# Kernel optimization log

Hardware: AMD Instinct MI355X
Metric: run time of the kernel (lower is better)

## Reference

```python
import jax, jax.numpy as jnp
import numpy as np

EMBED = 1024
HEADS = 16
HEAD_DIM = EMBED // HEADS
FFN = 4096
B, S = 2, 2048
EPS = 1e-5


def setup_inputs() -> dict:
    key = jax.random.key(0)
    ks = jax.random.split(key, 16)
    sc = 0.02
    return {
        "x": jax.random.normal(ks[0], (B, S, EMBED), jnp.float32),
        "rope_cos": jax.random.uniform(ks[1], (S, HEAD_DIM), jnp.float32),
        "rope_sin": jax.random.uniform(ks[2], (S, HEAD_DIM), jnp.float32),
        "Wq": jax.random.normal(ks[3], (EMBED, EMBED), jnp.float32) * sc,
        "bq": jnp.zeros((EMBED,), jnp.float32),
        "Wk": jax.random.normal(ks[4], (EMBED, EMBED), jnp.float32) * sc,
        "bk": jnp.zeros((EMBED,), jnp.float32),
        "Wv": jax.random.normal(ks[5], (EMBED, EMBED), jnp.float32) * sc,
        "bv": jnp.zeros((EMBED,), jnp.float32),
        "Wo": jax.random.normal(ks[6], (EMBED, EMBED), jnp.float32) * sc,
        "bo": jnp.zeros((EMBED,), jnp.float32),
        "W1": jax.random.normal(ks[7], (EMBED, FFN), jnp.float32) * sc,
        "b1": jnp.zeros((FFN,), jnp.float32),
        "W2": jax.random.normal(ks[8], (FFN, EMBED), jnp.float32) * sc,
        "b2": jnp.zeros((EMBED,), jnp.float32),
        "g1": jnp.ones((EMBED,), jnp.float32),
        "be1": jnp.zeros((EMBED,), jnp.float32),
        "g2": jnp.ones((EMBED,), jnp.float32),
        "be2": jnp.zeros((EMBED,), jnp.float32),
    }


def _layernorm(x, g, b):
    mu = jnp.mean(x, axis=-1, keepdims=True)
    var = jnp.var(x, axis=-1, keepdims=True)
    return (x - mu) * jax.lax.rsqrt(var + EPS) * g + b


def _rotate_half(x):
    half = x.shape[-1] // 2
    return jnp.concatenate((-x[..., half:], x[..., :half]), axis=-1)


def _apply_rope(x, cos, sin):
    # x: (B, H, S, D); cos/sin: (S, D)
    return x * cos[None, None] + _rotate_half(x) * sin[None, None]


def reference(x, rope_cos, rope_sin, Wq, bq, Wk, bk, Wv, bv, Wo, bo,
              W1, b1, W2, b2, g1, be1, g2, be2):
    batch, seq_len, embed = x.shape
    n = _layernorm(x, g1, be1)

    def heads(t):
        return t.reshape(batch, seq_len, HEADS, HEAD_DIM).transpose(0, 2, 1, 3)

    q = heads(n @ Wq + bq)
    k = heads(n @ Wk + bk)
    v = heads(n @ Wv + bv)
    q = _apply_rope(q, rope_cos, rope_sin)
    k = _apply_rope(k, rope_cos, rope_sin)

    scale = 1.0 / np.sqrt(HEAD_DIM)
    scores = jnp.einsum("bhqd,bhkd->bhqk", q, k) * scale  # (B,H,S,S)
    causal = jnp.triu(jnp.ones((seq_len, seq_len), bool), k=1)
    scores = jnp.where(causal[None, None], -jnp.inf, scores)
    attn = jax.nn.softmax(scores, axis=-1)
    out = jnp.einsum("bhqk,bhkd->bhqd", attn, v)
    out = out.transpose(0, 2, 1, 3).reshape(batch, seq_len, embed)
    x = x + (out @ Wo + bo)

    n2 = _layernorm(x, g2, be2)
    h = jax.nn.gelu(n2 @ W1 + b1, approximate=False)
    x = x + (h @ W2 + b2)
    return x
```

## Files before the change

### kernel.cpp

```cpp
#include <hip/hip_runtime.h>
#include <math.h>

#define EMBED 1024
#define SLEN  2048
#define BATCH 2
#define HEADS 16
#define HD    64
#define FFN_D 4096
#define MROWS (BATCH*SLEN)

typedef short bh8  __attribute__((ext_vector_type(8)));
typedef float f32x4 __attribute__((ext_vector_type(4)));

#define MFMA16(a,b,c) __builtin_amdgcn_mfma_f32_16x16x32_bf16((a),(b),(c),0,0,0)
#define GLDS16(g,l) __builtin_amdgcn_global_load_lds( \
    (__attribute__((address_space(1))) void*)(g), \
    (__attribute__((address_space(3))) void*)(l), 16, 0, 0)

__device__ inline float b2f(short s) {
  union { unsigned u; float f; } c; c.u = ((unsigned)(unsigned short)s) << 16; return c.f;
}
__device__ inline short f2b(float f) {
  union { float f; unsigned u; } c; c.f = f;
  unsigned r = (c.u + 0x7FFFu + ((c.u >> 16) & 1u)) >> 16;
  return (short)r;
}

__global__ __launch_bounds__(256) void transpose_w(const float* __restrict__ in,
                                                   short* __restrict__ out,
                                                   int K, int N) {
  __shared__ short sm[64][65];
  const int tid = threadIdx.x;
  const int k0 = blockIdx.y * 64, n0 = blockIdx.x * 64;
#pragma unroll
  for (int it = 0; it < 16; ++it) {
    int idx = it * 256 + tid;
    int r = idx >> 6, c = idx & 63;
    sm[r][c] = f2b(in[(size_t)(k0 + r) * N + n0 + c]);
  }
  __syncthreads();
#pragma unroll
  for (int it = 0; it < 16; ++it) {
    int idx = it * 256 + tid;
    int r = idx >> 6, c = idx & 63;
    out[(size_t)(n0 + r) * K + k0 + c] = sm[c][r];
  }
}

__global__ __launch_bounds__(256) void transpose_v(const short* __restrict__ in,
                                                   short* __restrict__ out) {
  __shared__ short sm[64][65];
  const int tid = threadIdx.x;
  const int s0 = blockIdx.x * 64, bh = blockIdx.y;
  const int b = bh >> 4, h = bh & 15;
#pragma unroll
  for (int it = 0; it < 16; ++it) {
    int idx = it * 256 + tid;
    int r = idx >> 6, c = idx & 63;
    sm[r][c] = in[((size_t)(b*SLEN + s0 + r))*EMBED + h*HD + c];
  }
  __syncthreads();
#pragma unroll
  for (int it = 0; it < 16; ++it) {
    int idx = it * 256 + tid;
    int r = idx >> 6, c = idx & 63;
    out[((size_t)(bh*HD + r))*SLEN + s0 + c] = sm[c][r];
  }
}

__global__ __launch_bounds__(256) void ln_kernel(const float* __restrict__ inF,
                                                 const short* __restrict__ inB,
                                                 const float* __restrict__ gw,
                                                 const float* __restrict__ bw,
                                                 short* __restrict__ out) {
  const int row = blockIdx.x, tid = threadIdx.x;
  const int w = tid >> 6;
  const size_t base = (size_t)row * EMBED;
  float x[4];
#pragma unroll
  for (int i = 0; i < 4; ++i) {
    int c = tid + i * 256;
    x[i] = inF ? inF[base + c] : b2f(inB[base + c]);
  }
  float s = x[0] + x[1] + x[2] + x[3];
  float ss = x[0]*x[0] + x[1]*x[1] + x[2]*x[2] + x[3]*x[3];
#pragma unroll
  for (int off = 32; off >= 1; off >>= 1) { s += __shfl_xor(s, off); ss += __shfl_xor(ss, off); }
  __shared__ float red[8];
  if ((tid & 63) == 0) { red[w*2] = s; red[w*2+1] = ss; }
  __syncthreads();
  s  = red[0] + red[2] + red[4] + red[6];
  ss = red[1] + red[3] + red[5] + red[7];
  const float mu = s * (1.0f/EMBED);
  const float var = ss * (1.0f/EMBED) - mu*mu;
  const float rstd = rsqrtf(var + 1e-5f);
#pragma unroll
  for (int i = 0; i < 4; ++i) {
    int c = tid + i * 256;
    out[base + c] = f2b((x[i]-mu)*rstd*gw[c] + bw[c]);
  }
}

__global__ __launch_bounds__(256) void rope_kernel(short* __restrict__ Qb, short* __restrict__ Kb,
                                                   const float* __restrict__ cosb,
                                                   const float* __restrict__ sinb) {
  const int idx = blockIdx.x * 256 + threadIdx.x;
  const int d = idx & 31;
  const int h = (idx >> 5) & 15;
  const int s = (idx >> 9) & 2047;
  const int b = idx >> 20;
  const size_t base = ((size_t)(b*SLEN + s))*EMBED + h*HD;
  const float c0 = cosb[s*HD + d],      s0 = sinb[s*HD + d];
  const float c1 = cosb[s*HD + 32 + d], s1 = sinb[s*HD + 32 + d];
  float q0 = b2f(Qb[base + d]), q1 = b2f(Qb[base + 32 + d]);
  Qb[base + d]      = f2b(q0*c0 - q1*s0);
  Qb[base + 32 + d] = f2b(q1*c1 + q0*s1);
  float k0 = b2f(Kb[base + d]), k1 = b2f(Kb[base + 32 + d]);
  Kb[base + d]      = f2b(k0*c0 - k1*s0);
  Kb[base + 32 + d] = f2b(k1*c1 + k0*s1);
}

__global__ __launch_bounds__(256) void gemm_bt(const short* __restrict__ A,
                                               const short* __restrict__ Bt,
                                               const float* __restrict__ bias0,
                                               const float* __restrict__ bias1,
                                               const float* __restrict__ bias2,
                                               float* __restrict__ outF,
                                               short* __restrict__ outB0,
                                               short* __restrict__ outB1,
                                               short* __restrict__ outB2,
                                               const float* __restrict__ residF,
                                               const short* __restrict__ residB,
                                               int N, int K, int gelu, int qkv) {
  __shared__ short As[128*32];
  __shared__ short Bs[128*32];
  const int tid = threadIdx.x;
  const int w = tid >> 6, L = tid & 63;
  const int quad = L >> 4, l16 = L & 15;
  const int bm = blockIdx.y * 128, bn = blockIdx.x * 128;
  const int wm = (w >> 1) * 64, wn = (w & 1) * 64;

  f32x4 acc[4][4];
#pragma unroll
  for (int i = 0; i < 4; ++i)
#pragma unroll
    for (int j = 0; j < 4; ++j) acc[i][j] = (f32x4){0.f,0.f,0.f,0.f};

  const int c0 = w*64 + L, c1 = 256 + w*64 + L;
  const short* a0p = A  + (size_t)(bm + (c0 >> 2))*K + (c0 & 3)*8;
  const short* a1p = A  + (size_t)(bm + (c1 >> 2))*K + (c1 & 3)*8;
  const short* b0p = Bt + (size_t)(bn + (c0 >> 2))*K + (c0 & 3)*8;
  const short* b1p = Bt + (size_t)(bn + (c1 >> 2))*K + (c1 & 3)*8;

  for (int k0 = 0; k0 < K; k0 += 32) {
    GLDS16(a0p + k0, As + w*512);
    GLDS16(a1p + k0, As + 2048 + w*512);
    GLDS16(b0p + k0, Bs + w*512);
    GLDS16(b1p + k0, Bs + 2048 + w*512);
    __syncthreads();
    bh8 af[4], bf[4];
#pragma unroll
    for (int mi = 0; mi < 4; ++mi)
      af[mi] = *(const bh8*)(As + (wm + mi*16 + l16)*32 + quad*8);
#pragma unroll
    for (int ni = 0; ni < 4; ++ni)
      bf[ni] = *(const bh8*)(Bs + (wn + ni*16 + l16)*32 + quad*8);
#pragma unroll
    for (int mi = 0; mi < 4; ++mi)
#pragma unroll
      for (int ni = 0; ni < 4; ++ni)
        acc[mi][ni] = MFMA16(af[mi], bf[ni], acc[mi][ni]);
    __syncthreads();
  }

#pragma unroll
  for (int mi = 0; mi < 4; ++mi) {
#pragma unroll
    for (int ni = 0; ni < 4; ++ni) {
      const int col = bn + wn + ni*16 + l16;
      float bv; short* ob; int colw; size_t rstride;
      if (qkv) {
        const int cc = col >> 10;
        colw = col & 1023;
        bv = (cc == 0 ? bias0 : cc == 1 ? bias1 : bias2)[colw];
        ob = (cc == 0 ? outB0 : cc == 1 ? outB1 : outB2);
        rstride = 1024;
      } else {
        colw = col; bv = bias0 ? bias0[col] : 0.f; ob = outB0; rstride = N;
      }
#pragma unroll
      for (int r = 0; r < 4; ++r) {
        const int gr = bm + wm + mi*16 + quad*4 + r;
        float v = acc[mi][ni][r] + bv;
        if (gelu) v = 0.5f*v*(1.f + erff(v*0.70710678f));
        if (residF) v += residF[(size_t)gr*N + col];
        if (residB) v += b2f(residB[(size_t)gr*N + col]);
        if (outF) outF[(size_t)gr*N + col] = v;
        if (ob)   ob[(size_t)gr*rstride + colw] = f2b(v);
      }
    }
  }
}

__global__ __launch_bounds__(256) void attn_kernel(const short* __restrict__ Qb,
                                                   const short* __restrict__ Kb,
                                                   const short* __restrict__ VT,
                                                   short* __restrict__ AOb) {
  __shared__ short Klds[64*72];
  __shared__ short Vlds[64*72];
  __shared__ short Plds[4*16*72];
  const int tid = threadIdx.x;
  const int w = tid >> 6, L = tid & 63, quad = L >> 4, l16 = L & 15;
  const int bh = blockIdx.x, qt = 31 - (int)blockIdx.y;
  const int b = bh >> 4, h = bh & 15;
  const int qbase = qt*64 + w*16;

  const size_t qrow = ((size_t)(b*SLEN + qbase + l16))*EMBED + h*HD;
  const bh8 aq0 = *(const bh8*)(Qb + qrow + quad*8);
  const bh8 aq1 = *(const bh8*)(Qb + qrow + 32 + quad*8);

  f32x4 o[4];
#pragma unroll
  for (int i = 0; i < 4; ++i) o[i] = (f32x4){0.f,0.f,0.f,0.f};
  float m_r[4] = {-1e30f,-1e30f,-1e30f,-1e30f};
  float l_r[4] = {0.f,0.f,0.f,0.f};
  const float scale = 0.125f;
  const size_t kg = ((size_t)(b*SLEN))*EMBED + h*HD;
  const size_t vg = ((size_t)(bh*HD))*SLEN;
  const int r0 = tid >> 3, ch = tid & 7;

  for (int kt = 0; kt <= qt; ++kt) {
    const int k0 = kt*64;
    __syncthreads();
    *(bh8*)(Klds + r0*72 + ch*8)      = *(const bh8*)(Kb + kg + (size_t)(k0 + r0)*EMBED + ch*8);
    *(bh8*)(Klds + (r0+32)*72 + ch*8) = *(const bh8*)(Kb + kg + (size_t)(k0 + r0 + 32)*EMBED + ch*8);
    *(bh8*)(Vlds + r0*72 + ch*8)      = *(const bh8*)(VT + vg + (size_t)r0*SLEN + k0 + ch*8);
    *(bh8*)(Vlds + (r0+32)*72 + ch*8) = *(const bh8*)(VT + vg + (size_t)(r0+32)*SLEN + k0 + ch*8);
    __syncthreads();

    f32x4 s[4];
#pragma unroll
    for (int nt = 0; nt < 4; ++nt) {
      s[nt] = (f32x4){0.f,0.f,0.f,0.f};
      const short* kp = Klds + (nt*16 + l16)*72 + quad*8;
      s[nt] = MFMA16(aq0, *(const bh8*)kp,        s[nt]);
      s[nt] = MFMA16(aq1, *(const bh8*)(kp + 32), s[nt]);
    }

    const bool lastTile = (kt == qt);
#pragma unroll
    for (int r = 0; r < 4; ++r) {
      const int q = qbase + quad*4 + r;
      float v[4];
#pragma unroll
      for (int nt = 0; nt < 4; ++nt) {
        v[nt] = s[nt][r]*scale;
        if (lastTile && (k0 + nt*16 + l16 > q)) v[nt] = -1e30f;
      }
      float mx = fmaxf(fmaxf(v[0], v[1]), fmaxf(v[2], v[3]));
#pragma unroll
      for (int off = 8; off >= 1; off >>= 1) mx = fmaxf(mx, __shfl_xor(mx, off));
      const float mnew = fmaxf(m_r[r], mx);
      const float alpha = __expf(m_r[r] - mnew);
      float p[4], rs = 0.f;
#pragma unroll
      for (int nt = 0; nt < 4; ++nt) { p[nt] = __expf(v[nt] - mnew); rs += p[nt]; }
#pragma unroll
      for (int off = 8; off >= 1; off >>= 1) rs += __shfl_xor(rs, off);
      l_r[r] = l_r[r]*alpha + rs;
      m_r[r] = mnew;
#pragma unroll
      for (int dt = 0; dt < 4; ++dt) o[dt][r] *= alpha;
      short* prow = Plds + w*1152 + (quad*4 + r)*72;
#pragma unroll
      for (int nt = 0; nt < 4; ++nt) prow[nt*16 + l16] = f2b(p[nt]);
    }

    const short* pr = Plds + w*1152 + l16*72;
    const bh8 pf0 = *(const bh8*)(pr + quad*8);
    const bh8 pf1 = *(const bh8*)(pr + 32 + quad*8);
#pragma unroll
    for (int dt = 0; dt < 4; ++dt) {
      const short* vp = Vlds + (dt*16 + l16)*72 + quad*8;
      o[dt] = MFMA16(pf0, *(const bh8*)vp,        o[dt]);
      o[dt] = MFMA16(pf1, *(const bh8*)(vp + 32), o[dt]);
    }
  }

#pragma unroll
  for (int r = 0; r < 4; ++r) {
    const float inv = 1.0f / l_r[r];
    const size_t orow = ((size_t)(b*SLEN + qbase + quad*4 + r))*EMBED + h*HD;
#pragma unroll
    for (int dt = 0; dt < 4; ++dt)
      AOb[orow + dt*16 + l16] = f2b(o[dt][r]*inv);
  }
}

extern "C" void kernel_launch(void* const* d_in, const int* in_sizes, int n_in,
                              void* d_out, int out_size, void* d_ws, size_t ws_size,
                              hipStream_t stream) {
  const float* x    = (const float*)d_in[0];
  const float* cosb = (const float*)d_in[1];
  const float* sinb = (const float*)d_in[2];
  const float* Wq = (const float*)d_in[3];  const float* bq  = (const float*)d_in[4];
  const float* Wk = (const float*)d_in[5];  const float* bk  = (const float*)d_in[6];
  const float* Wv = (const float*)d_in[7];  const float* bv  = (const float*)d_in[8];
  const float* Wo = (const float*)d_in[9];  const float* bo  = (const float*)d_in[10];
  const float* W1 = (const float*)d_in[11]; const float* b1  = (const float*)d_in[12];
  const float* W2 = (const float*)d_in[13]; const float* b2  = (const float*)d_in[14];
  const float* g1 = (const float*)d_in[15]; const float* be1 = (const float*)d_in[16];
  const float* g2 = (const float*)d_in[17]; const float* be2 = (const float*)d_in[18];
  float* out = (float*)d_out;

  char* ws = (char*)d_ws;
  const size_t MB = 1ull << 20;
  short* wqkvT = (short*)(ws + 0*MB);
  short* woT = (short*)(ws + 6*MB);
  short* w2T = (short*)(ws + 0*MB);
  short* w1T = (short*)(ws + 8*MB);
  short* n1b = (short*)(ws + 16*MB);
  short* Qb  = (short*)(ws + 24*MB);
  short* Kb  = (short*)(ws + 32*MB);
  short* Vb  = (short*)(ws + 40*MB);
  short* AOb = (short*)(ws + 48*MB);
  short* VTb = (short*)(ws + 56*MB);
  short* X1b = (short*)(ws + 16*MB);
  short* n2b = (short*)(ws + 24*MB);
  short* Hb  = (short*)(ws + 32*MB);

  transpose_w<<<dim3(16,16), 256, 0, stream>>>(Wq, wqkvT,                1024, 1024);
  transpose_w<<<dim3(16,16), 256, 0, stream>>>(Wk, wqkvT + 1024*1024,    1024, 1024);
  transpose_w<<<dim3(16,16), 256, 0, stream>>>(Wv, wqkvT + 2*1024*1024,  1024, 1024);
  transpose_w<<<dim3(16,16), 256, 0, stream>>>(Wo, woT, 1024, 1024);
  transpose_w<<<dim3(64,16), 256, 0, stream>>>(W1, w1T, 1024, 4096);

  ln_kernel<<<MROWS, 256, 0, stream>>>(x, nullptr, g1, be1, n1b);

  gemm_bt<<<dim3(24,32), 256, 0, stream>>>(n1b, wqkvT, bq, bk, bv,
                                           nullptr, Qb, Kb, Vb, nullptr, nullptr,
                                           3072, 1024, 0, 1);

  rope_kernel<<<8192, 256, 0, stream>>>(Qb, Kb, cosb, sinb);

  transpose_v<<<dim3(32,32), 256, 0, stream>>>(Vb, VTb);

  attn_kernel<<<dim3(32,32), 256, 0, stream>>>(Qb, Kb, VTb, AOb);

  gemm_bt<<<dim3(8,32), 256, 0, stream>>>(AOb, woT, bo, nullptr, nullptr,
                                          nullptr, X1b, nullptr, nullptr, x, nullptr,
                                          1024, 1024, 0, 0);

  transpose_w<<<dim3(16,64), 256, 0, stream>>>(W2, w2T, 4096, 1024);

  ln_kernel<<<MROWS, 256, 0, stream>>>(nullptr, X1b, g2, be2, n2b);

  gemm_bt<<<dim3(32,32), 256, 0, stream>>>(n2b, w1T, b1, nullptr, nullptr,
                                           nullptr, Hb, nullptr, nullptr, nullptr, nullptr,
                                           4096, 1024, 1, 0);

  gemm_bt<<<dim3(8,32), 256, 0, stream>>>(Hb, w2T, b2, nullptr, nullptr,
                                          out, nullptr, nullptr, nullptr, nullptr, X1b,
                                          1024, 4096, 0, 0);
}
```

Before: 505.0 us.

## Split-K the Wo and W2 GEMMs with atomic accumulation into fp32 output

Adds a split-K mode to gemm_bt. Each z-slice computes a K-chunk and atomically adds its partial tile into an fp32 output that a new init_out kernel pre-fills with residual plus bias. The Wo GEMM uses 2 splits and the W2 GEMM uses 4, raising grid occupancy from 256 blocks to 512 and 1024. The residual X1 is now kept in fp32 instead of bf16, and the workspace layout and W2 transpose placement are reshuffled. The cost is atomic traffic, extra init passes and non-deterministic summation order.

```diff
diff --git a/kernel.cpp b/kernel.cpp
--- a/kernel.cpp
+++ b/kernel.cpp
@@ -120,6 +120,16 @@
   Kb[base + 32 + d] = f2b(k1*c1 + k0*s1);
 }
 
+__global__ __launch_bounds__(256) void init_out(const float* __restrict__ bias,
+                                                const float* __restrict__ resid,
+                                                float* __restrict__ out) {
+  const int idx = blockIdx.x * 256 + threadIdx.x;
+  f32x4 r = ((const f32x4*)resid)[idx];
+  const int c = (idx << 2) & 1023;
+  r[0] += bias[c]; r[1] += bias[c+1]; r[2] += bias[c+2]; r[3] += bias[c+3];
+  ((f32x4*)out)[idx] = r;
+}
+
 __global__ __launch_bounds__(256) void gemm_bt(const short* __restrict__ A,
                                                const short* __restrict__ Bt,
                                                const float* __restrict__ bias0,
@@ -131,7 +141,8 @@
                                                short* __restrict__ outB2,
                                                const float* __restrict__ residF,
                                                const short* __restrict__ residB,
-                                               int N, int K, int gelu, int qkv) {
+                                               int N, int K, int gelu, int qkv,
+                                               int kChunk) {
   __shared__ short As[128*32];
   __shared__ short Bs[128*32];
   const int tid = threadIdx.x;
@@ -139,6 +150,8 @@
   const int quad = L >> 4, l16 = L & 15;
   const int bm = blockIdx.y * 128, bn = blockIdx.x * 128;
   const int wm = (w >> 1) * 64, wn = (w & 1) * 64;
+  const int kS = kChunk ? (int)blockIdx.z * kChunk : 0;
+  const int kE = kChunk ? kS + kChunk : K;
 
   f32x4 acc[4][4];
 #pragma unroll
@@ -152,7 +165,7 @@
   const short* b0p = Bt + (size_t)(bn + (c0 >> 2))*K + (c0 & 3)*8;
   const short* b1p = Bt + (size_t)(bn + (c1 >> 2))*K + (c1 & 3)*8;
 
-  for (int k0 = 0; k0 < K; k0 += 32) {
+  for (int k0 = kS; k0 < kE; k0 += 32) {
     GLDS16(a0p + k0, As + w*512);
     GLDS16(a1p + k0, As + 2048 + w*512);
     GLDS16(b0p + k0, Bs + w*512);
@@ -173,6 +186,20 @@
     __syncthreads();
   }
 
+  if (kChunk) {
+#pragma unroll
+    for (int mi = 0; mi < 4; ++mi)
+#pragma unroll
+      for (int ni = 0; ni < 4; ++ni) {
+        const int col = bn + wn + ni*16 + l16;
+#pragma unroll
+        for (int r = 0; r < 4; ++r) {
+          const int gr = bm + wm + mi*16 + quad*4 + r;
+          atomicAdd(outF + (size_t)gr*N + col, acc[mi][ni][r]);
+        }
+      }
+    return;
+  }
 #pragma unroll
   for (int mi = 0; mi < 4; ++mi) {
 #pragma unroll
@@ -317,17 +344,17 @@
   const size_t MB = 1ull << 20;
   short* wqkvT = (short*)(ws + 0*MB);
   short* woT = (short*)(ws + 6*MB);
-  short* w2T = (short*)(ws + 0*MB);
   short* w1T = (short*)(ws + 8*MB);
   short* n1b = (short*)(ws + 16*MB);
   short* Qb  = (short*)(ws + 24*MB);
   short* Kb  = (short*)(ws + 32*MB);
   short* Vb  = (short*)(ws + 40*MB);
-  short* AOb = (short*)(ws + 48*MB);
-  short* VTb = (short*)(ws + 56*MB);
-  short* X1b = (short*)(ws + 16*MB);
-  short* n2b = (short*)(ws + 24*MB);
+  short* VTb = (short*)(ws + 48*MB);
+  short* AOb = (short*)(ws + 56*MB);
+  float* X1f = (float*)(ws + 16*MB);
+  short* n2b = (short*)(ws + 0*MB);
   short* Hb  = (short*)(ws + 32*MB);
+  short* w2T = (short*)(ws + 0*MB);
 
   transpose_w<<<dim3(16,16), 256, 0, stream>>>(Wq, wqkvT,                1024, 1024);
   transpose_w<<<dim3(16,16), 256, 0, stream>>>(Wk, wqkvT + 1024*1024,    1024, 1024);
@@ -339,7 +366,7 @@
 
   gemm_bt<<<dim3(24,32), 256, 0, stream>>>(n1b, wqkvT, bq, bk, bv,
                                            nullptr, Qb, Kb, Vb, nullptr, nullptr,
-                                           3072, 1024, 0, 1);
+                                           3072, 1024, 0, 1, 0);
 
   rope_kernel<<<8192, 256, 0, stream>>>(Qb, Kb, cosb, sinb);
 
@@ -347,19 +374,21 @@
 
   attn_kernel<<<dim3(32,32), 256, 0, stream>>>(Qb, Kb, VTb, AOb);
 
-  gemm_bt<<<dim3(8,32), 256, 0, stream>>>(AOb, woT, bo, nullptr, nullptr,
-                                          nullptr, X1b, nullptr, nullptr, x, nullptr,
-                                          1024, 1024, 0, 0);
-
-  transpose_w<<<dim3(16,64), 256, 0, stream>>>(W2, w2T, 4096, 1024);
-
-  ln_kernel<<<MROWS, 256, 0, stream>>>(nullptr, X1b, g2, be2, n2b);
+  init_out<<<4096, 256, 0, stream>>>(bo, x, X1f);
+  gemm_bt<<<dim3(8,32,2), 256, 0, stream>>>(AOb, woT, nullptr, nullptr, nullptr,
+                                            X1f, nullptr, nullptr, nullptr, nullptr, nullptr,
+                                            1024, 1024, 0, 0, 512);
+
+  ln_kernel<<<MROWS, 256, 0, stream>>>(X1f, nullptr, g2, be2, n2b);
 
   gemm_bt<<<dim3(32,32), 256, 0, stream>>>(n2b, w1T, b1, nullptr, nullptr,
                                            nullptr, Hb, nullptr, nullptr, nullptr, nullptr,
-                                           4096, 1024, 1, 0);
-
-  gemm_bt<<<dim3(8,32), 256, 0, stream>>>(Hb, w2T, b2, nullptr, nullptr,
-                                          out, nullptr, nullptr, nullptr, nullptr, X1b,
-                                          1024, 4096, 0, 0);
-}
+                                           4096, 1024, 1, 0, 0);
+
+  transpose_w<<<dim3(16,64), 256, 0, stream>>>(W2, w2T, 4096, 1024);
+
+  init_out<<<4096, 256, 0, stream>>>(b2, X1f, out);
+  gemm_bt<<<dim3(8,32,4), 256, 0, stream>>>(Hb, w2T, nullptr, nullptr, nullptr,
+                                            out, nullptr, nullptr, nullptr, nullptr, nullptr,
+                                            1024, 4096, 0, 0, 1024);
+}
```

After: 512.6 us. Within noise of the previous version (+1.5%).

## Pipeline GEMM with double-buffered LDS, swizzled layout, and workgroup remapping

Applied to the files above, without the earlier changes.

Rewrites the bf16 GEMM main loop to process a 64-wide K tile per iteration across two LDS buffers. Global-to-LDS loads run two tiles ahead, gated by explicit vmcnt waits and raw barriers, so memory traffic overlaps MFMA work. LDS rows use an XOR swizzle to reduce bank conflicts, and block indices are remapped for better L2 locality. The residual stream after attention is now kept in fp32 rather than bf16, and the workspace is rearranged. This adds LDS use (64KB per block) and depends on hand-written wait counts being exactly right.

```diff
diff --git a/kernel.cpp b/kernel.cpp
--- a/kernel.cpp
+++ b/kernel.cpp
@@ -11,11 +11,14 @@
 
 typedef short bh8  __attribute__((ext_vector_type(8)));
 typedef float f32x4 __attribute__((ext_vector_type(4)));
+typedef __attribute__((address_space(3))) const short* lsp;
 
 #define MFMA16(a,b,c) __builtin_amdgcn_mfma_f32_16x16x32_bf16((a),(b),(c),0,0,0)
 #define GLDS16(g,l) __builtin_amdgcn_global_load_lds( \
     (__attribute__((address_space(1))) void*)(g), \
     (__attribute__((address_space(3))) void*)(l), 16, 0, 0)
+#define DSR(dst, base, IMM) \
+  asm volatile("ds_read_b128 %0, %1 offset:" #IMM : "=v"(dst) : "v"(base))
 
 __device__ inline float b2f(short s) {
   union { unsigned u; float f; } c; c.u = ((unsigned)(unsigned short)s) << 16; return c.f;
@@ -120,25 +123,35 @@
   Kb[base + 32 + d] = f2b(k1*c1 + k0*s1);
 }
 
-__global__ __launch_bounds__(256) void gemm_bt(const short* __restrict__ A,
-                                               const short* __restrict__ Bt,
-                                               const float* __restrict__ bias0,
-                                               const float* __restrict__ bias1,
-                                               const float* __restrict__ bias2,
-                                               float* __restrict__ outF,
-                                               short* __restrict__ outB0,
-                                               short* __restrict__ outB1,
-                                               short* __restrict__ outB2,
-                                               const float* __restrict__ residF,
-                                               const short* __restrict__ residB,
-                                               int N, int K, int gelu, int qkv) {
-  __shared__ short As[128*32];
-  __shared__ short Bs[128*32];
+__global__ __launch_bounds__(256, 2) void gemm_bt(const short* __restrict__ A,
+                                                  const short* __restrict__ Bt,
+                                                  const float* __restrict__ bias0,
+                                                  const float* __restrict__ bias1,
+                                                  const float* __restrict__ bias2,
+                                                  float* __restrict__ outF,
+                                                  short* __restrict__ outB0,
+                                                  short* __restrict__ outB1,
+                                                  short* __restrict__ outB2,
+                                                  const float* __restrict__ residF,
+                                                  const short* __restrict__ residB,
+                                                  int N, int K, int gelu, int qkv) {
+  __shared__ short As[16384];
+  __shared__ short Bs[16384];
   const int tid = threadIdx.x;
   const int w = tid >> 6, L = tid & 63;
   const int quad = L >> 4, l16 = L & 15;
-  const int bm = blockIdx.y * 128, bn = blockIdx.x * 128;
+
+  int bx = blockIdx.x, by = blockIdx.y;
+  {
+    const int gx = gridDim.x;
+    const int nwg = gx * gridDim.y;
+    const int wg = by*gx + bx;
+    const int swz = (wg & 7)*(nwg >> 3) + (wg >> 3);
+    bx = swz % gx; by = swz / gx;
+  }
+  const int bm = by * 128, bn = bx * 128;
   const int wm = (w >> 1) * 64, wn = (w & 1) * 64;
+  const int NT = K >> 6;
 
   f32x4 acc[4][4];
 #pragma unroll
@@ -146,47 +159,95 @@
 #pragma unroll
     for (int j = 0; j < 4; ++j) acc[i][j] = (f32x4){0.f,0.f,0.f,0.f};
 
-  const int c0 = w*64 + L, c1 = 256 + w*64 + L;
-  const short* a0p = A  + (size_t)(bm + (c0 >> 2))*K + (c0 & 3)*8;
-  const short* a1p = A  + (size_t)(bm + (c1 >> 2))*K + (c1 & 3)*8;
-  const short* b0p = Bt + (size_t)(bn + (c0 >> 2))*K + (c0 & 3)*8;
-  const short* b1p = Bt + (size_t)(bn + (c1 >> 2))*K + (c1 & 3)*8;
-
-  for (int k0 = 0; k0 < K; k0 += 32) {
-    GLDS16(a0p + k0, As + w*512);
-    GLDS16(a1p + k0, As + 2048 + w*512);
-    GLDS16(b0p + k0, Bs + w*512);
-    GLDS16(b1p + k0, Bs + 2048 + w*512);
-    __syncthreads();
+  const int c0i = tid, c1i = 256 + tid;
+  const int r0i = c0i >> 2, s0i = (c0i & 3) ^ ((r0i >> 1) & 3);
+  const int r1i = c1i >> 2, s1i = (c1i & 3) ^ ((r1i >> 1) & 3);
+  const short* aG0 = A  + (size_t)(bm + r0i)*K + s0i*8;
+  const short* aG1 = A  + (size_t)(bm + r1i)*K + s1i*8;
+  const short* bG0 = Bt + (size_t)(bn + r0i)*K + s0i*8;
+  const short* bG1 = Bt + (size_t)(bn + r1i)*K + s1i*8;
+
+  const int ssw = (l16 >> 1) & 3;
+  lsp pA0 = (lsp)(As + (wm + l16)*32 + ((quad ^ ssw) << 3));
+  lsp pB0 = (lsp)(Bs + (wn + l16)*32 + ((quad ^ ssw) << 3));
+  lsp pA1 = pA0 + 8192;
+  lsp pB1 = pB0 + 8192;
+
+#define STG(DST, G0, G1, BUF, KH, KOFF) do { \
+    GLDS16(G0 + (KOFF) + (KH)*32, DST + (BUF)*8192 + (KH)*4096 + w*512); \
+    GLDS16(G1 + (KOFF) + (KH)*32, DST + (BUF)*8192 + (KH)*4096 + 2048 + w*512); \
+  } while (0)
+
+  STG(As, aG0, aG1, 0, 0, 0);   STG(Bs, bG0, bG1, 0, 0, 0);
+  STG(As, aG0, aG1, 0, 1, 0);   STG(Bs, bG0, bG1, 0, 1, 0);
+  STG(As, aG0, aG1, 1, 0, 64);  STG(Bs, bG0, bG1, 1, 0, 64);
+  STG(As, aG0, aG1, 1, 1, 64);  STG(Bs, bG0, bG1, 1, 1, 64);
+
+  for (int t = 0; t < NT; ++t) {
+    const int cb = t & 1;
+    lsp Ab = cb ? pA1 : pA0;
+    lsp Bb = cb ? pB1 : pB0;
+    const bool pf = (t + 2) < NT;
+    const int kofA = (t + 2) << 6;
     bh8 af[4], bf[4];
-#pragma unroll
-    for (int mi = 0; mi < 4; ++mi)
-      af[mi] = *(const bh8*)(As + (wm + mi*16 + l16)*32 + quad*8);
-#pragma unroll
-    for (int ni = 0; ni < 4; ++ni)
-      bf[ni] = *(const bh8*)(Bs + (wn + ni*16 + l16)*32 + quad*8);
+
+    if (t < NT-1) asm volatile("s_waitcnt vmcnt(12)" ::: "memory");
+    else          asm volatile("s_waitcnt vmcnt(4)"  ::: "memory");
+    __builtin_amdgcn_s_barrier();
+    DSR(af[0], Ab, 0);    DSR(af[1], Ab, 1024);
+    DSR(af[2], Ab, 2048); DSR(af[3], Ab, 3072);
+    DSR(bf[0], Bb, 0);    DSR(bf[1], Bb, 1024);
+    DSR(bf[2], Bb, 2048); DSR(bf[3], Bb, 3072);
+    asm volatile("s_waitcnt lgkmcnt(0)" ::: "memory");
+    __builtin_amdgcn_sched_barrier(0);
+    __builtin_amdgcn_s_barrier();
+    if (pf) { STG(As, aG0, aG1, cb, 0, kofA); STG(Bs, bG0, bG1, cb, 0, kofA); }
+    __builtin_amdgcn_sched_barrier(0);
+    __builtin_amdgcn_s_setprio(1);
 #pragma unroll
     for (int mi = 0; mi < 4; ++mi)
 #pragma unroll
       for (int ni = 0; ni < 4; ++ni)
         acc[mi][ni] = MFMA16(af[mi], bf[ni], acc[mi][ni]);
-    __syncthreads();
-  }
+    __builtin_amdgcn_s_setprio(0);
+
+    if (t < NT-2)       asm volatile("s_waitcnt vmcnt(12)" ::: "memory");
+    else if (t == NT-2) asm volatile("s_waitcnt vmcnt(8)"  ::: "memory");
+    else                asm volatile("s_waitcnt vmcnt(0)"  ::: "memory");
+    __builtin_amdgcn_s_barrier();
+    DSR(af[0], Ab, 8192);  DSR(af[1], Ab, 9216);
+    DSR(af[2], Ab, 10240); DSR(af[3], Ab, 11264);
+    DSR(bf[0], Bb, 8192);  DSR(bf[1], Bb, 9216);
+    DSR(bf[2], Bb, 10240); DSR(bf[3], Bb, 11264);
+    asm volatile("s_waitcnt lgkmcnt(0)" ::: "memory");
+    __builtin_amdgcn_sched_barrier(0);
+    __builtin_amdgcn_s_barrier();
+    if (pf) { STG(As, aG0, aG1, cb, 1, kofA); STG(Bs, bG0, bG1, cb, 1, kofA); }
+    __builtin_amdgcn_sched_barrier(0);
+    __builtin_amdgcn_s_setprio(1);
+#pragma unroll
+    for (int mi = 0; mi < 4; ++mi)
+#pragma unroll
+      for (int ni = 0; ni < 4; ++ni)
+        acc[mi][ni] = MFMA16(af[mi], bf[ni], acc[mi][ni]);
+    __builtin_amdgcn_s_setprio(0);
+  }
+#undef STG
 
 #pragma unroll
   for (int mi = 0; mi < 4; ++mi) {
 #pragma unroll
     for (int ni = 0; ni < 4; ++ni) {
       const int col = bn + wn + ni*16 + l16;
-      float bv; short* ob; int colw; size_t rstride;
+      float bv; short* ob2; int colw; size_t rstride;
       if (qkv) {
         const int cc = col >> 10;
         colw = col & 1023;
         bv = (cc == 0 ? bias0 : cc == 1 ? bias1 : bias2)[colw];
-        ob = (cc == 0 ? outB0 : cc == 1 ? outB1 : outB2);
+        ob2 = (cc == 0 ? outB0 : cc == 1 ? outB1 : outB2);
         rstride = 1024;
       } else {
-        colw = col; bv = bias0 ? bias0[col] : 0.f; ob = outB0; rstride = N;
+        colw = col; bv = bias0 ? bias0[col] : 0.f; ob2 = outB0; rstride = N;
       }
 #pragma unroll
       for (int r = 0; r < 4; ++r) {
@@ -196,7 +257,7 @@
         if (residF) v += residF[(size_t)gr*N + col];
         if (residB) v += b2f(residB[(size_t)gr*N + col]);
         if (outF) outF[(size_t)gr*N + col] = v;
-        if (ob)   ob[(size_t)gr*rstride + colw] = f2b(v);
+        if (ob2)  ob2[(size_t)gr*rstride + colw] = f2b(v);
       }
     }
   }
@@ -317,17 +378,17 @@
   const size_t MB = 1ull << 20;
   short* wqkvT = (short*)(ws + 0*MB);
   short* woT = (short*)(ws + 6*MB);
-  short* w2T = (short*)(ws + 0*MB);
   short* w1T = (short*)(ws + 8*MB);
   short* n1b = (short*)(ws + 16*MB);
   short* Qb  = (short*)(ws + 24*MB);
   short* Kb  = (short*)(ws + 32*MB);
   short* Vb  = (short*)(ws + 40*MB);
-  short* AOb = (short*)(ws + 48*MB);
-  short* VTb = (short*)(ws + 56*MB);
-  short* X1b = (short*)(ws + 16*MB);
-  short* n2b = (short*)(ws + 24*MB);
+  short* VTb = (short*)(ws + 48*MB);
+  short* AOb = (short*)(ws + 56*MB);
+  float* X1f = (float*)(ws + 16*MB);
+  short* n2b = (short*)(ws + 0*MB);
   short* Hb  = (short*)(ws + 32*MB);
+  short* w2T = (short*)(ws + 0*MB);
 
   transpose_w<<<dim3(16,16), 256, 0, stream>>>(Wq, wqkvT,                1024, 1024);
   transpose_w<<<dim3(16,16), 256, 0, stream>>>(Wk, wqkvT + 1024*1024,    1024, 1024);
@@ -348,18 +409,18 @@
   attn_kernel<<<dim3(32,32), 256, 0, stream>>>(Qb, Kb, VTb, AOb);
 
   gemm_bt<<<dim3(8,32), 256, 0, stream>>>(AOb, woT, bo, nullptr, nullptr,
-                                          nullptr, X1b, nullptr, nullptr, x, nullptr,
+                                          X1f, nullptr, nullptr, nullptr, x, nullptr,
                                           1024, 1024, 0, 0);
 
-  transpose_w<<<dim3(16,64), 256, 0, stream>>>(W2, w2T, 4096, 1024);
-
-  ln_kernel<<<MROWS, 256, 0, stream>>>(nullptr, X1b, g2, be2, n2b);
+  ln_kernel<<<MROWS, 256, 0, stream>>>(X1f, nullptr, g2, be2, n2b);
 
   gemm_bt<<<dim3(32,32), 256, 0, stream>>>(n2b, w1T, b1, nullptr, nullptr,
                                            nullptr, Hb, nullptr, nullptr, nullptr, nullptr,
                                            4096, 1024, 1, 0);
 
+  transpose_w<<<dim3(16,64), 256, 0, stream>>>(W2, w2T, 4096, 1024);
+
   gemm_bt<<<dim3(8,32), 256, 0, stream>>>(Hb, w2T, b2, nullptr, nullptr,
-                                          out, nullptr, nullptr, nullptr, nullptr, X1b,
+                                          out, nullptr, nullptr, nullptr, X1f, nullptr,
                                           1024, 4096, 0, 0);
 }
```

Result: faster. 455.4 us (-9.8%).
